# Optimization experiments

Hardware: AMD Instinct MI355X
Metric: run time of the kernel (lower is better)

The kernel has to match this reference:

```python
import jax, jax.numpy as jnp
import numpy as np

D_MODEL = 512
NHEAD = 8
HEAD_DIM = D_MODEL // NHEAD
A, B = 1024, 16


def setup_inputs() -> dict:
    key = jax.random.key(0)
    ks = jax.random.split(key, 6)
    s = 1.0 / np.sqrt(D_MODEL)
    return {
        "src": jax.random.normal(ks[0], (A, B, D_MODEL), jnp.float32),
        "asset_relation_bias": jax.random.normal(ks[1], (A, A), jnp.float32) * 0.1,
        "Wq": jax.random.normal(ks[2], (D_MODEL, D_MODEL), jnp.float32) * s,
        "bq": jnp.zeros((D_MODEL,), jnp.float32),
        "Wk": jax.random.normal(ks[3], (D_MODEL, D_MODEL), jnp.float32) * s,
        "bk": jnp.zeros((D_MODEL,), jnp.float32),
        "Wv": jax.random.normal(ks[4], (D_MODEL, D_MODEL), jnp.float32) * s,
        "bv": jnp.zeros((D_MODEL,), jnp.float32),
        "Wo": jax.random.normal(ks[5], (D_MODEL, D_MODEL), jnp.float32) * s,
        "bo": jnp.zeros((D_MODEL,), jnp.float32),
    }


def reference(src, asset_relation_bias, Wq, bq, Wk, bk, Wv, bv, Wo, bo):
    # src: [A, B, H]; attention is over the asset dim A.
    scale = HEAD_DIM ** -0.5

    def proj_heads(x, W, b):
        y = x @ W.T + b                      # [A, B, H]  (torch Linear: x @ W.T + b)
        y = y.reshape(A, B, NHEAD, HEAD_DIM)
        return jnp.transpose(y, (1, 2, 0, 3))  # [B, nh, A, hd]

    q = proj_heads(src, Wq, bq)
    k = proj_heads(src, Wk, bk)
    v = proj_heads(src, Wv, bv)

    logits = jnp.einsum("bnad,bnkd->bnak", q, k) * scale  # [B, nh, A, A]
    logits = logits + asset_relation_bias[None, None]     # additive relation bias
    attn = jax.nn.softmax(logits, axis=-1)                # dropout = identity (eval)
    out = jnp.einsum("bnak,bnkd->bnad", attn, v)          # [B, nh, A, hd]
    out = jnp.transpose(out, (2, 0, 1, 3)).reshape(A, B, D_MODEL)
    out = out @ Wo.T + bo
    return out
```

## Files before the change

kernel.cpp:

```cpp
#include <hip/hip_runtime.h>
#include <hip/hip_bf16.h>

#define A_DIM 1024
#define B_DIM 16
#define DM    512
#define NH    8
#define HD    64
#define NTOK  (A_DIM * B_DIM)

#define LDT 72
#define LOG2E 1.44269504088896f

typedef short s16x8 __attribute__((ext_vector_type(8)));
typedef short s16x4 __attribute__((ext_vector_type(4)));
typedef float f32x4 __attribute__((ext_vector_type(4)));

static __device__ __forceinline__ unsigned short f2b(float f) {
    __hip_bfloat16 h = __float2bfloat16(f);
    unsigned short u;
    __builtin_memcpy(&u, &h, 2);
    return u;
}
static __device__ __forceinline__ unsigned int pk2(float a, float b) {
    __hip_bfloat162 h = __float22bfloat162_rn(make_float2(a, b));
    unsigned int u;
    __builtin_memcpy(&u, &h, 4);
    return u;
}
static __device__ __forceinline__ uint2 cvt4(float4 v) {
    return make_uint2(pk2(v.x, v.y), pk2(v.z, v.w));
}

__global__ __launch_bounds__(256) void bias_scale(
    const float* __restrict__ in, float* __restrict__ out)
{
    int i = (blockIdx.x * 256 + threadIdx.x) * 4;
    float4 v = *(const float4*)&in[i];
    v.x *= LOG2E; v.y *= LOG2E; v.z *= LOG2E; v.w *= LOG2E;
    *(float4*)&out[i] = v;
}

__global__ __launch_bounds__(256) void qkv_gemm(
    const float* __restrict__ src,
    const float* __restrict__ Wq, const float* __restrict__ bq,
    const float* __restrict__ Wk, const float* __restrict__ bk,
    const float* __restrict__ Wv, const float* __restrict__ bv,
    short* __restrict__ Qb, short* __restrict__ Kb, short* __restrict__ Vb)
{
    __shared__ short As[128 * LDT];
    __shared__ short Bs[128 * LDT];

    const int tid  = threadIdx.x;
    const int wave = tid >> 6, lane = tid & 63;
    const int quad = lane >> 4, l16 = lane & 15;
    const int waveM = (wave >> 1) * 64, waveN = (wave & 1) * 64;
    const int mbase = blockIdx.y * 128;
    const int nbase = blockIdx.x * 128;
    const int mat   = nbase >> 9;
    const float* W    = (mat == 0) ? Wq : (mat == 1) ? Wk : Wv;
    const float* bvec = (mat == 0) ? bq : (mat == 1) ? bk : bv;
    short* dst        = (mat == 0) ? Qb : (mat == 1) ? Kb : Vb;
    const float oscale = (mat == 0) ? 0.125f * LOG2E : 1.0f;
    const int wrow0 = nbase & 511;

    f32x4 acc[4][4];
    #pragma unroll
    for (int i = 0; i < 4; i++)
        #pragma unroll
        for (int j = 0; j < 4; j++)
            acc[i][j] = (f32x4){0.f, 0.f, 0.f, 0.f};

    for (int kb = 0; kb < 8; ++kb) {
        __syncthreads();
        #pragma unroll
        for (int p = 0; p < 8; p++) {
            int chunk = tid + p * 256;
            int row = chunk >> 4, c = chunk & 15;
            float4 a4 = *(const float4*)&src[(mbase + row) * 512 + kb * 64 + c * 4];
            *(uint2*)&As[row * LDT + c * 4] = cvt4(a4);
            float4 w4 = *(const float4*)&W[(wrow0 + row) * 512 + kb * 64 + c * 4];
            *(uint2*)&Bs[row * LDT + c * 4] = cvt4(w4);
        }
        __syncthreads();
        #pragma unroll
        for (int k0i = 0; k0i < 2; k0i++) {
            s16x8 af[4], bf[4];
            #pragma unroll
            for (int mi = 0; mi < 4; mi++)
                af[mi] = *(const s16x8*)&As[(waveM + mi * 16 + l16) * LDT + (k0i * 4 + quad) * 8];
            #pragma unroll
            for (int ni = 0; ni < 4; ni++)
                bf[ni] = *(const s16x8*)&Bs[(waveN + ni * 16 + l16) * LDT + (k0i * 4 + quad) * 8];
            #pragma unroll
            for (int mi = 0; mi < 4; mi++)
                #pragma unroll
                for (int ni = 0; ni < 4; ni++)
                    acc[mi][ni] = __builtin_amdgcn_mfma_f32_16x16x32_bf16(
                        af[mi], bf[ni], acc[mi][ni], 0, 0, 0);
        }
    }

    #pragma unroll
    for (int mi = 0; mi < 4; mi++) {
        #pragma unroll
        for (int ni = 0; ni < 4; ni++) {
            #pragma unroll
            for (int r = 0; r < 4; r++) {
                int t = mbase + waveM + mi * 16 + quad * 4 + r;
                int o = wrow0 + waveN + ni * 16 + l16;
                float v = (acc[mi][ni][r] + bvec[o]) * oscale;
                int a = t >> 4, bb = t & 15, n = o >> 6, d = o & 63;
                dst[((bb * NH + n) * A_DIM + a) * HD + d] = (short)f2b(v);
            }
        }
    }
}

__global__ __launch_bounds__(256) void attn_kernel(
    const short* __restrict__ Qb, const short* __restrict__ Kb,
    const short* __restrict__ Vb, const float* __restrict__ biasS,
    short* __restrict__ AO)
{
    __shared__ short Ks[2][64 * LDT];
    __shared__ short Vt[2][64 * LDT];

    const int tid  = threadIdx.x;
    const int lane = tid & 63;
    const int wave = tid >> 6;
    const int quad = lane >> 4, l16 = lane & 15;
    const int qh = quad >> 1, ql = quad & 1;
    const int bn = blockIdx.y;
    const int qrow0 = blockIdx.x * 64 + wave * 16;

    const short* Qg = Qb + bn * (A_DIM * HD);
    const short* Kg = Kb + bn * (A_DIM * HD);
    const short* Vg = Vb + bn * (A_DIM * HD);
    const float* brow = biasS + (size_t)(qrow0 + l16) * A_DIM;

    s16x8 qf[2];
    #pragma unroll
    for (int k0i = 0; k0i < 2; k0i++)
        qf[k0i] = *(const s16x8*)&Qg[(qrow0 + l16) * HD + k0i * 32 + quad * 8];

    const int row0 = tid >> 3, c0 = tid & 7;
    const int row1 = (tid + 256) >> 3, c1 = c0;

    float lsum = 0.f;
    f32x4 of[4];
    #pragma unroll
    for (int db = 0; db < 4; db++) of[db] = (f32x4){0.f, 0.f, 0.f, 0.f};

    {
        s16x8 k0 = *(const s16x8*)&Kg[row0 * HD + c0 * 8];
        s16x8 k1 = *(const s16x8*)&Kg[row1 * HD + c1 * 8];
        s16x8 v0 = *(const s16x8*)&Vg[row0 * HD + c0 * 8];
        s16x8 v1 = *(const s16x8*)&Vg[row1 * HD + c1 * 8];
        *(s16x8*)&Ks[0][row0 * LDT + c0 * 8] = k0;
        *(s16x8*)&Ks[0][row1 * LDT + c1 * 8] = k1;
        #pragma unroll
        for (int j = 0; j < 8; j++) {
            Vt[0][(c0 * 8 + j) * LDT + (((row0 >> 3) ^ c0) << 3) + (row0 & 7)] = v0[j];
            Vt[0][(c1 * 8 + j) * LDT + (((row1 >> 3) ^ c1) << 3) + (row1 & 7)] = v1[j];
        }
    }
    __syncthreads();

    for (int kb = 0; kb < 16; ++kb) {
        const int buf = kb & 1;

        s16x8 kp0, kp1, vp0, vp1;
        if (kb < 15) {
            const short* Kn = Kg + (kb + 1) * 64 * HD;
            const short* Vn = Vg + (kb + 1) * 64 * HD;
            kp0 = *(const s16x8*)&Kn[row0 * HD + c0 * 8];
            kp1 = *(const s16x8*)&Kn[row1 * HD + c1 * 8];
            vp0 = *(const s16x8*)&Vn[row0 * HD + c0 * 8];
            vp1 = *(const s16x8*)&Vn[row1 * HD + c1 * 8];
        }

        float pv[4][4];
        #pragma unroll
        for (int cb = 0; cb < 4; cb++) {
            f32x4 s = (f32x4){0.f, 0.f, 0.f, 0.f};
            #pragma unroll
            for (int k0i = 0; k0i < 2; k0i++) {
                s16x8 kf = *(const s16x8*)&Ks[buf][(cb * 16 + l16) * LDT + (k0i * 4 + quad) * 8];
                s = __builtin_amdgcn_mfma_f32_16x16x32_bf16(kf, qf[k0i], s, 0, 0, 0);
            }
            float4 bz = *(const float4*)&brow[kb * 64 + cb * 16 + quad * 4];
            pv[cb][0] = __builtin_exp2f(s[0] + bz.x);
            pv[cb][1] = __builtin_exp2f(s[1] + bz.y);
            pv[cb][2] = __builtin_exp2f(s[2] + bz.z);
            pv[cb][3] = __builtin_exp2f(s[3] + bz.w);
            lsum += pv[cb][0] + pv[cb][1] + pv[cb][2] + pv[cb][3];
        }

        uint4 ua = make_uint4(pk2(pv[0][0], pv[0][1]), pk2(pv[0][2], pv[0][3]),
                              pk2(pv[1][0], pv[1][1]), pk2(pv[1][2], pv[1][3]));
        uint4 ub = make_uint4(pk2(pv[2][0], pv[2][1]), pk2(pv[2][2], pv[2][3]),
                              pk2(pv[3][0], pv[3][1]), pk2(pv[3][2], pv[3][3]));
        s16x8 pfA, pfB;
        __builtin_memcpy(&pfA, &ua, 16);
        __builtin_memcpy(&pfB, &ub, 16);

        #pragma unroll
        for (int db = 0; db < 4; db++) {
            int dd = db * 16 + l16, d3 = dd >> 3;
            int base = dd * LDT + ql * 4;
            s16x4 v0 = *(const s16x4*)&Vt[buf][base + (((0 + qh) ^ d3) << 3)];
            s16x4 v1 = *(const s16x4*)&Vt[buf][base + (((2 + qh) ^ d3) << 3)];
            s16x8 vf01 = __builtin_shufflevector(v0, v1, 0, 1, 2, 3, 4, 5, 6, 7);
            of[db] = __builtin_amdgcn_mfma_f32_16x16x32_bf16(pfA, vf01, of[db], 0, 0, 0);
            s16x4 v2 = *(const s16x4*)&Vt[buf][base + (((4 + qh) ^ d3) << 3)];
            s16x4 v3 = *(const s16x4*)&Vt[buf][base + (((6 + qh) ^ d3) << 3)];
            s16x8 vf23 = __builtin_shufflevector(v2, v3, 0, 1, 2, 3, 4, 5, 6, 7);
            of[db] = __builtin_amdgcn_mfma_f32_16x16x32_bf16(pfB, vf23, of[db], 0, 0, 0);
        }

        if (kb < 15) {
            const int nb = buf ^ 1;
            *(s16x8*)&Ks[nb][row0 * LDT + c0 * 8] = kp0;
            *(s16x8*)&Ks[nb][row1 * LDT + c1 * 8] = kp1;
            #pragma unroll
            for (int j = 0; j < 8; j++) {
                Vt[nb][(c0 * 8 + j) * LDT + (((row0 >> 3) ^ c0) << 3) + (row0 & 7)] = vp0[j];
                Vt[nb][(c1 * 8 + j) * LDT + (((row1 >> 3) ^ c1) << 3) + (row1 & 7)] = vp1[j];
            }
        }
        __syncthreads();
    }

    lsum += __shfl_xor(lsum, 16);
    lsum += __shfl_xor(lsum, 32);
    float linv[4];
    #pragma unroll
    for (int r = 0; r < 4; r++)
        linv[r] = 1.0f / __shfl(lsum, (lane & 48) | (quad * 4 + r));

    const int b = bn >> 3, n = bn & 7;
    #pragma unroll
    for (int db = 0; db < 4; db++) {
        #pragma unroll
        for (int r = 0; r < 4; r++) {
            int a = qrow0 + quad * 4 + r;
            int d = db * 16 + l16;
            AO[(a * B_DIM + b) * DM + n * HD + d] = (short)f2b(of[db][r] * linv[r]);
        }
    }
}

__global__ __launch_bounds__(256) void out_gemm(
    const short* __restrict__ Xin,
    const float* __restrict__ Wo, const float* __restrict__ bo,
    float* __restrict__ out)
{
    __shared__ short As[128 * LDT];
    __shared__ short Bs[128 * LDT];

    const int tid  = threadIdx.x;
    const int wave = tid >> 6, lane = tid & 63;
    const int quad = lane >> 4, l16 = lane & 15;
    const int waveM = (wave >> 1) * 64, waveN = (wave & 1) * 64;
    const int mbase = blockIdx.y * 128;
    const int nbase = blockIdx.x * 128;

    f32x4 acc[4][4];
    #pragma unroll
    for (int i = 0; i < 4; i++)
        #pragma unroll
        for (int j = 0; j < 4; j++)
            acc[i][j] = (f32x4){0.f, 0.f, 0.f, 0.f};

    for (int kb = 0; kb < 8; ++kb) {
        __syncthreads();
        #pragma unroll
        for (int p = 0; p < 4; p++) {
            int chunk = tid + p * 256;
            int row = chunk >> 3, c = chunk & 7;
            *(s16x8*)&As[row * LDT + c * 8] =
                *(const s16x8*)&Xin[(mbase + row) * 512 + kb * 64 + c * 8];
        }
        #pragma unroll
        for (int p = 0; p < 8; p++) {
            int chunk = tid + p * 256;
            int row = chunk >> 4, c = chunk & 15;
            float4 w4 = *(const float4*)&Wo[(nbase + row) * 512 + kb * 64 + c * 4];
            *(uint2*)&Bs[row * LDT + c * 4] = cvt4(w4);
        }
        __syncthreads();
        #pragma unroll
        for (int k0i = 0; k0i < 2; k0i++) {
            s16x8 af[4], bf[4];
            #pragma unroll
            for (int mi = 0; mi < 4; mi++)
                af[mi] = *(const s16x8*)&As[(waveM + mi * 16 + l16) * LDT + (k0i * 4 + quad) * 8];
            #pragma unroll
            for (int ni = 0; ni < 4; ni++)
                bf[ni] = *(const s16x8*)&Bs[(waveN + ni * 16 + l16) * LDT + (k0i * 4 + quad) * 8];
            #pragma unroll
            for (int mi = 0; mi < 4; mi++)
                #pragma unroll
                for (int ni = 0; ni < 4; ni++)
                    acc[mi][ni] = __builtin_amdgcn_mfma_f32_16x16x32_bf16(
                        af[mi], bf[ni], acc[mi][ni], 0, 0, 0);
        }
    }

    #pragma unroll
    for (int mi = 0; mi < 4; mi++) {
        #pragma unroll
        for (int ni = 0; ni < 4; ni++) {
            #pragma unroll
            for (int r = 0; r < 4; r++) {
                int t = mbase + waveM + mi * 16 + quad * 4 + r;
                int o = nbase + waveN + ni * 16 + l16;
                out[t * 512 + o] = acc[mi][ni][r] + bo[o];
            }
        }
    }
}

extern "C" void kernel_launch(void* const* d_in, const int* in_sizes, int n_in,
                              void* d_out, int out_size, void* d_ws, size_t ws_size,
                              hipStream_t stream) {
    const float* src  = (const float*)d_in[0];
    const float* bias = (const float*)d_in[1];
    const float* Wq   = (const float*)d_in[2];
    const float* bq   = (const float*)d_in[3];
    const float* Wk   = (const float*)d_in[4];
    const float* bk   = (const float*)d_in[5];
    const float* Wv   = (const float*)d_in[6];
    const float* bv   = (const float*)d_in[7];
    const float* Wo   = (const float*)d_in[8];
    const float* bo   = (const float*)d_in[9];

    short* ws = (short*)d_ws;
    short* Qb = ws;
    short* Kb = ws + (size_t)(1 << 23);
    short* Vb = ws + (size_t)(2 << 23);

    const bool big_ws = ws_size >= (size_t)(72u << 20);
    float* biasS;
    short* AO;
    if (big_ws) {
        biasS = (float*)(ws + (size_t)3 * (1 << 23));
        AO    = ws + (size_t)3 * (1 << 23) + (size_t)(1 << 21);
    } else {
        AO    = (short*)d_out;
        biasS = (float*)((short*)d_out + (size_t)NTOK * DM);
    }

    bias_scale<<<dim3(A_DIM * A_DIM / 1024), 256, 0, stream>>>(bias, biasS);
    qkv_gemm<<<dim3(12, 128), 256, 0, stream>>>(src, Wq, bq, Wk, bk, Wv, bv, Qb, Kb, Vb);
    attn_kernel<<<dim3(16, 128), 256, 0, stream>>>(Qb, Kb, Vb, biasS, AO);

    if (big_ws) {
        out_gemm<<<dim3(4, 128), 256, 0, stream>>>(AO, Wo, bo, (float*)d_out);
    } else {
        float* Cs = (float*)d_ws;
        out_gemm<<<dim3(4, 128), 256, 0, stream>>>(AO, Wo, bo, Cs);
        (void)hipMemcpyAsync(d_out, Cs, (size_t)out_size * sizeof(float),
                             hipMemcpyDeviceToDevice, stream);
    }
}
```

Before: 262.6 us.

## Pre-swizzle V and K into MFMA fragment order, store bias as bf16

Adds a v_transpose kernel that rewrites V in place into MFMA B-fragment order, and has the attention kernel stage K and V into shared memory in fragment-major layout. Each lane now does single 16-byte LDS reads and writes, replacing the scalar transposing stores and split 8-byte loads. The relation bias is pre-scaled and stored as bf16 to halve its read traffic, at some precision cost. The loop barrier also moves to the top of each iteration. The price is an extra kernel launch plus one more read and write pass over V.

```diff
diff --git a/kernel.cpp b/kernel.cpp
--- a/kernel.cpp
+++ b/kernel.cpp
@@ -21,6 +21,12 @@
     __builtin_memcpy(&u, &h, 2);
     return u;
 }
+static __device__ __forceinline__ float b2f(unsigned short u) {
+    unsigned int w = ((unsigned int)u) << 16;
+    float f;
+    __builtin_memcpy(&f, &w, 4);
+    return f;
+}
 static __device__ __forceinline__ unsigned int pk2(float a, float b) {
     __hip_bfloat162 h = __float22bfloat162_rn(make_float2(a, b));
     unsigned int u;
@@ -32,12 +38,12 @@
 }
 
 __global__ __launch_bounds__(256) void bias_scale(
-    const float* __restrict__ in, float* __restrict__ out)
+    const float* __restrict__ in, short* __restrict__ out)
 {
     int i = (blockIdx.x * 256 + threadIdx.x) * 4;
     float4 v = *(const float4*)&in[i];
-    v.x *= LOG2E; v.y *= LOG2E; v.z *= LOG2E; v.w *= LOG2E;
-    *(float4*)&out[i] = v;
+    uint2 u = cvt4(make_float4(v.x * LOG2E, v.y * LOG2E, v.z * LOG2E, v.w * LOG2E));
+    *(uint2*)&out[i] = u;
 }
 
 __global__ __launch_bounds__(256) void qkv_gemm(
@@ -116,34 +122,65 @@
     }
 }
 
+__global__ __launch_bounds__(256) void v_transpose(short* __restrict__ V)
+{
+    __shared__ short Lt[64 * LDT];
+
+    const int tid = threadIdx.x;
+    short* T = V + ((size_t)blockIdx.y * (A_DIM * HD)) + blockIdx.x * 64 * HD;
+
+    #pragma unroll
+    for (int p = 0; p < 2; p++) {
+        int chunk = tid + p * 256;
+        int row = chunk >> 3, c = chunk & 7;
+        *(s16x8*)&Lt[row * LDT + c * 8] = *(const s16x8*)&T[row * 64 + c * 8];
+    }
+    __syncthreads();
+
+    #pragma unroll
+    for (int p = 0; p < 2; p++) {
+        int id = tid + p * 256;
+        int s = id >> 6, lane = id & 63;
+        int quad = lane >> 4, l16 = lane & 15;
+        int db = s >> 1, pr = s & 1;
+        int d = db * 16 + l16;
+        int k0 = pr * 32 + quad * 4;
+        s16x8 o;
+        #pragma unroll
+        for (int i = 0; i < 4; i++) o[i]     = Lt[(k0 + i) * LDT + d];
+        #pragma unroll
+        for (int i = 0; i < 4; i++) o[4 + i] = Lt[(k0 + 16 + i) * LDT + d];
+        *(s16x8*)&T[(s * 64 + lane) * 8] = o;
+    }
+}
+
 __global__ __launch_bounds__(256) void attn_kernel(
     const short* __restrict__ Qb, const short* __restrict__ Kb,
-    const short* __restrict__ Vb, const float* __restrict__ biasS,
+    const short* __restrict__ Vt, const short* __restrict__ bias16,
     short* __restrict__ AO)
 {
-    __shared__ short Ks[2][64 * LDT];
-    __shared__ short Vt[2][64 * LDT];
+    __shared__ short KsF[2][8 * 512];
+    __shared__ short VsF[2][8 * 512];
 
     const int tid  = threadIdx.x;
-    const int lane = tid & 63;
-    const int wave = tid >> 6;
+    const int wave = tid >> 6, lane = tid & 63;
     const int quad = lane >> 4, l16 = lane & 15;
-    const int qh = quad >> 1, ql = quad & 1;
     const int bn = blockIdx.y;
     const int qrow0 = blockIdx.x * 64 + wave * 16;
 
-    const short* Qg = Qb + bn * (A_DIM * HD);
-    const short* Kg = Kb + bn * (A_DIM * HD);
-    const short* Vg = Vb + bn * (A_DIM * HD);
-    const float* brow = biasS + (size_t)(qrow0 + l16) * A_DIM;
+    const short* Qg = Qb + (size_t)bn * (A_DIM * HD);
+    const short* Kg = Kb + (size_t)bn * (A_DIM * HD);
+    const short* Vg = Vt + (size_t)bn * (A_DIM * HD);
+    const short* brow = bias16 + (size_t)(qrow0 + l16) * A_DIM;
 
     s16x8 qf[2];
     #pragma unroll
     for (int k0i = 0; k0i < 2; k0i++)
         qf[k0i] = *(const s16x8*)&Qg[(qrow0 + l16) * HD + k0i * 32 + quad * 8];
 
-    const int row0 = tid >> 3, c0 = tid & 7;
-    const int row1 = (tid + 256) >> 3, c1 = c0;
+    const short* kga = Kg + (wave * 16 + l16) * HD + quad * 8;
+    const short* vga = Vg + wave * 1024 + lane * 8;
+    const int sk = wave * 2;
 
     float lsum = 0.f;
     f32x4 of[4];
@@ -151,48 +188,46 @@
     for (int db = 0; db < 4; db++) of[db] = (f32x4){0.f, 0.f, 0.f, 0.f};
 
     {
-        s16x8 k0 = *(const s16x8*)&Kg[row0 * HD + c0 * 8];
-        s16x8 k1 = *(const s16x8*)&Kg[row1 * HD + c1 * 8];
-        s16x8 v0 = *(const s16x8*)&Vg[row0 * HD + c0 * 8];
-        s16x8 v1 = *(const s16x8*)&Vg[row1 * HD + c1 * 8];
-        *(s16x8*)&Ks[0][row0 * LDT + c0 * 8] = k0;
-        *(s16x8*)&Ks[0][row1 * LDT + c1 * 8] = k1;
-        #pragma unroll
-        for (int j = 0; j < 8; j++) {
-            Vt[0][(c0 * 8 + j) * LDT + (((row0 >> 3) ^ c0) << 3) + (row0 & 7)] = v0[j];
-            Vt[0][(c1 * 8 + j) * LDT + (((row1 >> 3) ^ c1) << 3) + (row1 & 7)] = v1[j];
-        }
-    }
-    __syncthreads();
+        s16x8 k0 = *(const s16x8*)(kga);
+        s16x8 k1 = *(const s16x8*)(kga + 32);
+        s16x8 v0 = *(const s16x8*)(vga);
+        s16x8 v1 = *(const s16x8*)(vga + 512);
+        *(s16x8*)&KsF[0][(sk + 0) * 512 + lane * 8] = k0;
+        *(s16x8*)&KsF[0][(sk + 1) * 512 + lane * 8] = k1;
+        *(s16x8*)&VsF[0][(sk + 0) * 512 + lane * 8] = v0;
+        *(s16x8*)&VsF[0][(sk + 1) * 512 + lane * 8] = v1;
+    }
 
     for (int kb = 0; kb < 16; ++kb) {
         const int buf = kb & 1;
+        __syncthreads();
 
         s16x8 kp0, kp1, vp0, vp1;
         if (kb < 15) {
-            const short* Kn = Kg + (kb + 1) * 64 * HD;
-            const short* Vn = Vg + (kb + 1) * 64 * HD;
-            kp0 = *(const s16x8*)&Kn[row0 * HD + c0 * 8];
-            kp1 = *(const s16x8*)&Kn[row1 * HD + c1 * 8];
-            vp0 = *(const s16x8*)&Vn[row0 * HD + c0 * 8];
-            vp1 = *(const s16x8*)&Vn[row1 * HD + c1 * 8];
+            const short* kn = kga + (kb + 1) * 4096;
+            const short* vn = vga + (kb + 1) * 4096;
+            kp0 = *(const s16x8*)(kn);
+            kp1 = *(const s16x8*)(kn + 32);
+            vp0 = *(const s16x8*)(vn);
+            vp1 = *(const s16x8*)(vn + 512);
         }
 
         float pv[4][4];
         #pragma unroll
         for (int cb = 0; cb < 4; cb++) {
-            f32x4 s = (f32x4){0.f, 0.f, 0.f, 0.f};
+            f32x4 st = (f32x4){0.f, 0.f, 0.f, 0.f};
             #pragma unroll
             for (int k0i = 0; k0i < 2; k0i++) {
-                s16x8 kf = *(const s16x8*)&Ks[buf][(cb * 16 + l16) * LDT + (k0i * 4 + quad) * 8];
-                s = __builtin_amdgcn_mfma_f32_16x16x32_bf16(kf, qf[k0i], s, 0, 0, 0);
+                s16x8 kf = *(const s16x8*)&KsF[buf][(cb * 2 + k0i) * 512 + lane * 8];
+                st = __builtin_amdgcn_mfma_f32_16x16x32_bf16(kf, qf[k0i], st, 0, 0, 0);
             }
-            float4 bz = *(const float4*)&brow[kb * 64 + cb * 16 + quad * 4];
-            pv[cb][0] = __builtin_exp2f(s[0] + bz.x);
-            pv[cb][1] = __builtin_exp2f(s[1] + bz.y);
-            pv[cb][2] = __builtin_exp2f(s[2] + bz.z);
-            pv[cb][3] = __builtin_exp2f(s[3] + bz.w);
-            lsum += pv[cb][0] + pv[cb][1] + pv[cb][2] + pv[cb][3];
+            s16x4 bz = *(const s16x4*)&brow[kb * 64 + cb * 16 + quad * 4];
+            #pragma unroll
+            for (int r = 0; r < 4; r++) {
+                float p = __builtin_exp2f(st[r] + b2f((unsigned short)bz[r]));
+                pv[cb][r] = p;
+                lsum += p;
+            }
         }
 
         uint4 ua = make_uint4(pk2(pv[0][0], pv[0][1]), pk2(pv[0][2], pv[0][3]),
@@ -205,29 +240,19 @@
 
         #pragma unroll
         for (int db = 0; db < 4; db++) {
-            int dd = db * 16 + l16, d3 = dd >> 3;
-            int base = dd * LDT + ql * 4;
-            s16x4 v0 = *(const s16x4*)&Vt[buf][base + (((0 + qh) ^ d3) << 3)];
-            s16x4 v1 = *(const s16x4*)&Vt[buf][base + (((2 + qh) ^ d3) << 3)];
-            s16x8 vf01 = __builtin_shufflevector(v0, v1, 0, 1, 2, 3, 4, 5, 6, 7);
-            of[db] = __builtin_amdgcn_mfma_f32_16x16x32_bf16(pfA, vf01, of[db], 0, 0, 0);
-            s16x4 v2 = *(const s16x4*)&Vt[buf][base + (((4 + qh) ^ d3) << 3)];
-            s16x4 v3 = *(const s16x4*)&Vt[buf][base + (((6 + qh) ^ d3) << 3)];
-            s16x8 vf23 = __builtin_shufflevector(v2, v3, 0, 1, 2, 3, 4, 5, 6, 7);
-            of[db] = __builtin_amdgcn_mfma_f32_16x16x32_bf16(pfB, vf23, of[db], 0, 0, 0);
+            s16x8 v0 = *(const s16x8*)&VsF[buf][(db * 2 + 0) * 512 + lane * 8];
+            of[db] = __builtin_amdgcn_mfma_f32_16x16x32_bf16(pfA, v0, of[db], 0, 0, 0);
+            s16x8 v1 = *(const s16x8*)&VsF[buf][(db * 2 + 1) * 512 + lane * 8];
+            of[db] = __builtin_amdgcn_mfma_f32_16x16x32_bf16(pfB, v1, of[db], 0, 0, 0);
         }
 
         if (kb < 15) {
             const int nb = buf ^ 1;
-            *(s16x8*)&Ks[nb][row0 * LDT + c0 * 8] = kp0;
-            *(s16x8*)&Ks[nb][row1 * LDT + c1 * 8] = kp1;
-            #pragma unroll
-            for (int j = 0; j < 8; j++) {
-                Vt[nb][(c0 * 8 + j) * LDT + (((row0 >> 3) ^ c0) << 3) + (row0 & 7)] = vp0[j];
-                Vt[nb][(c1 * 8 + j) * LDT + (((row1 >> 3) ^ c1) << 3) + (row1 & 7)] = vp1[j];
-            }
-        }
-        __syncthreads();
+            *(s16x8*)&KsF[nb][(sk + 0) * 512 + lane * 8] = kp0;
+            *(s16x8*)&KsF[nb][(sk + 1) * 512 + lane * 8] = kp1;
+            *(s16x8*)&VsF[nb][(sk + 0) * 512 + lane * 8] = vp0;
+            *(s16x8*)&VsF[nb][(sk + 1) * 512 + lane * 8] = vp1;
+        }
     }
 
     lsum += __shfl_xor(lsum, 16);
@@ -244,7 +269,7 @@
         for (int r = 0; r < 4; r++) {
             int a = qrow0 + quad * 4 + r;
             int d = db * 16 + l16;
-            AO[(a * B_DIM + b) * DM + n * HD + d] = (short)f2b(of[db][r] * linv[r]);
+            AO[((size_t)a * B_DIM + b) * DM + n * HD + d] = (short)f2b(of[db][r] * linv[r]);
         }
     }
 }
@@ -340,19 +365,20 @@
     short* Vb = ws + (size_t)(2 << 23);
 
     const bool big_ws = ws_size >= (size_t)(72u << 20);
-    float* biasS;
     short* AO;
+    short* bias16;
     if (big_ws) {
-        biasS = (float*)(ws + (size_t)3 * (1 << 23));
-        AO    = ws + (size_t)3 * (1 << 23) + (size_t)(1 << 21);
+        AO     = ws + (size_t)3 * (1 << 23);
+        bias16 = ws + (size_t)4 * (1 << 23);
     } else {
-        AO    = (short*)d_out;
-        biasS = (float*)((short*)d_out + (size_t)NTOK * DM);
-    }
-
-    bias_scale<<<dim3(A_DIM * A_DIM / 1024), 256, 0, stream>>>(bias, biasS);
+        AO     = (short*)d_out;
+        bias16 = (short*)d_out + (size_t)(1 << 23);
+    }
+
+    bias_scale<<<dim3(1024), 256, 0, stream>>>(bias, bias16);
     qkv_gemm<<<dim3(12, 128), 256, 0, stream>>>(src, Wq, bq, Wk, bk, Wv, bv, Qb, Kb, Vb);
-    attn_kernel<<<dim3(16, 128), 256, 0, stream>>>(Qb, Kb, Vb, biasS, AO);
+    v_transpose<<<dim3(16, 128), 256, 0, stream>>>(Vb);
+    attn_kernel<<<dim3(16, 128), 256, 0, stream>>>(Qb, Kb, Vb, bias16, AO);
 
     if (big_ws) {
         out_gemm<<<dim3(4, 128), 256, 0, stream>>>(AO, Wo, bo, (float*)d_out);
```

Measured after the change: 284.9 us. 1.08x slower.
